# Performance work log

Hardware: AMD Instinct MI355X
Metric: run time of the kernel (lower is better)

The kernel has to match this reference:

```python
import jax, jax.numpy as jnp
import numpy as np

NODES_PER_GRAPH = 1430  # hard-coded stride in the original forward
GENE0 = 1421            # first gene node index per graph
N_HEADS = 9


def gcn_conv(x, W, b, src, dst, n):
    """PyG-style GCNConv: D^-1/2 (A+I) D^-1/2 X W + b (self-loops added)."""
    h = x @ W  # [N, out]
    ones = jnp.ones(src.shape, jnp.float32)
    deg = jax.ops.segment_sum(ones, dst, num_segments=n) + 1.0  # +1 self-loop
    dinv = jax.lax.rsqrt(deg)
    norm = dinv[src] * dinv[dst]  # [E]
    agg = jax.ops.segment_sum(norm[:, None] * h[src], dst, num_segments=n)
    agg = agg + (dinv * dinv)[:, None] * h  # self-loop contribution
    return agg + b


def setup_inputs() -> dict:
    key = jax.random.key(0)
    ks = jax.random.split(key, 8)
    n_graphs = 512
    n = NODES_PER_GRAPH * n_graphs  # 732160 nodes
    e = n * 8                        # avg degree 8
    x = jax.random.normal(ks[0], (n, 1), jnp.float32)
    edge_index = jax.random.randint(ks[1], (2, e), 0, n, jnp.int32)
    y = jnp.zeros((n_graphs * N_HEADS,), jnp.int32)  # only y.size(0) is used
    W1 = jax.random.normal(ks[2], (1, 16), jnp.float32) * 0.5
    b1 = jnp.zeros((16,), jnp.float32)
    W2 = jax.random.normal(ks[3], (16, 16), jnp.float32) * 0.25
    b2 = jnp.zeros((16,), jnp.float32)
    fw1 = jax.random.normal(ks[4], (N_HEADS, 16, 8), jnp.float32) * 0.25
    fb1 = jnp.zeros((N_HEADS, 8), jnp.float32)
    fw2 = jax.random.normal(ks[5], (N_HEADS, 8, 1), jnp.float32) * 0.35
    fb2 = jnp.zeros((N_HEADS, 1), jnp.float32)
    return {"x": x, "edge_index": edge_index, "y": y, "W1": W1, "b1": b1,
            "W2": W2, "b2": b2, "fw1": fw1, "fb1": fb1, "fw2": fw2, "fb2": fb2}


def reference(x, edge_index, y, W1, b1, W2, b2, fw1, fb1, fw2, fb2):
    n = x.shape[0]
    src, dst = edge_index[0], edge_index[1]
    h = jax.nn.relu(gcn_conv(x, W1, b1, src, dst, n))
    # F.dropout(p=0.4) treated as identity (deterministic eval reference)
    h = jax.nn.relu(gcn_conv(h, W2, b2, src, dst, n))
    n_graphs = y.shape[0] // N_HEADS
    # fused version of the per-gene gather loop: idx[g, k] = 1421+g + k*1430
    idx = (GENE0 + jnp.arange(N_HEADS)[:, None]
           + jnp.arange(n_graphs)[None, :] * NODES_PER_GRAPH)  # [9, G]
    g = h[idx]  # [9, G, 16]
    z = jax.nn.relu(jnp.einsum('gnf,gfh->gnh', g, fw1) + fb1[:, None, :])
    pred = jnp.einsum('gnh,gho->gno', z, fw2) + fb2[:, None, :]  # [9, G, 1]
    return tuple(pred[i] for i in range(N_HEADS))
```

## Files before the change

kernel.cpp:

```cpp
#include <hip/hip_runtime.h>

#define NODES 1430
#define GENE0 1421
#define NHEADS 9
#define BHIST 1024
#define GMAX 64
#define QCAP 1024

__device__ __forceinline__ float frelu(float v) { return v > 0.f ? v : 0.f; }

__global__ __launch_bounds__(BHIST, 4)
void k_hist(const int* __restrict__ esrc, const int* __restrict__ edst,
            unsigned int* __restrict__ copies,
            int* __restrict__ gene_cnt, int* __restrict__ gene_src,
            unsigned int* __restrict__ flagw,
            int e, int K, int R, int n, int hbins, int hwords) {
    extern __shared__ unsigned int lds[];
    int id = blockIdx.x;
    int k, r;
    if ((K & 7) == 0) {
        int xcd = id & 7;
        int slot = id >> 3;
        int cin = slot / R;
        k = xcd * (K >> 3) + cin;
        r = slot - cin * R;
    } else {
        k = id / R;
        r = id - k * R;
    }
    const int tid = threadIdx.x;
    {
        uint4* l4 = (uint4*)lds;
        const int hw4 = hwords >> 2;
        for (int w = tid; w < hw4; w += BHIST) l4[w] = make_uint4(0, 0, 0, 0);
    }
    __syncthreads();

    const unsigned int lo = (unsigned int)r * (unsigned int)hbins;
    const unsigned int hb = (unsigned int)hbins;
    const int e4 = e >> 2;
    const int Q = (e4 + K - 1) / K;
    const int beg = k * Q;
    const int end = min(beg + Q, e4);
    const int4* ed4 = (const int4*)edst;
    const int len = (end > beg) ? (end - beg) : 0;
    const int eighth = len >> 3;

    auto proc = [&](int4 d4) {
#pragma unroll
        for (int c = 0; c < 4; c++) {
            unsigned int d = (unsigned int)((&d4.x)[c]);
            unsigned int rel = d - lo;
            if (rel < hb)
                atomicAdd(&lds[rel >> 3], 1u << ((rel & 7u) * 4u));
        }
    };

    for (int i = tid; i < eighth; i += BHIST) {
        int j0 = beg + i;
        int4 v0 = ed4[j0];
        int4 v1 = ed4[j0 + eighth];
        int4 v2 = ed4[j0 + 2 * eighth];
        int4 v3 = ed4[j0 + 3 * eighth];
        int4 v4 = ed4[j0 + 4 * eighth];
        int4 v5 = ed4[j0 + 5 * eighth];
        int4 v6 = ed4[j0 + 6 * eighth];
        int4 v7 = ed4[j0 + 7 * eighth];
        proc(v0); proc(v1); proc(v2); proc(v3);
        proc(v4); proc(v5); proc(v6); proc(v7);
    }
    for (int i = (eighth << 3) + tid; i < len; i += BHIST) {
        proc(ed4[beg + i]);
    }

    {
        int sbeg = beg + (int)(((long long)len * r) / R);
        int send = beg + (int)(((long long)len * (r + 1)) / R);
        for (int j = sbeg + tid; j < send; j += BHIST) {
            int4 d4 = ed4[j];
#pragma unroll
            for (int c = 0; c < 4; c++) {
                unsigned int d = (unsigned int)((&d4.x)[c]);
                unsigned int graph = d / NODES;
                unsigned int pos = d - graph * NODES;
                if (pos >= GENE0) {
                    int s = esrc[4 * j + c];
                    atomicOr(&flagw[(unsigned)s >> 5], 1u << (s & 31));
                    int g = (int)(graph * NHEADS + (pos - GENE0));
                    int p = atomicAdd(gene_cnt + g, 1);
                    if (p < GMAX) gene_src[(g << 6) + p] = s;
                }
            }
        }
    }

    if (k == 0) {
        for (int j = (e4 << 2) + tid; j < e; j += BHIST) {
            unsigned int d = (unsigned int)edst[j];
            unsigned int rel = d - lo;
            if (rel < hb)
                atomicAdd(&lds[rel >> 3], 1u << ((rel & 7u) * 4u));
            if (r == 0) {
                unsigned int graph = d / NODES;
                unsigned int pos = d - graph * NODES;
                if (pos >= GENE0) {
                    int s = esrc[j];
                    atomicOr(&flagw[(unsigned)s >> 5], 1u << (s & 31));
                    int g = (int)(graph * NHEADS + (pos - GENE0));
                    int p = atomicAdd(gene_cnt + g, 1);
                    if (p < GMAX) gene_src[(g << 6) + p] = s;
                }
            }
        }
    }
    __syncthreads();
    int wlimit = (n > (int)lo) ? ((n - (int)lo + 7) >> 3) : 0;
    if (wlimit > hwords) wlimit = hwords;
    int w4 = (wlimit + 3) >> 2;
    uint4* dst4 = (uint4*)(copies + ((size_t)k * R + r) * hwords);
    const uint4* l4 = (const uint4*)lds;
    for (int w = tid; w < w4; w += BHIST) dst4[w] = l4[w];
}

__global__ void k_reduce(const unsigned int* __restrict__ copies,
                         const float* __restrict__ x,
                         float2* __restrict__ dx, float* __restrict__ t,
                         unsigned int* __restrict__ flagw,
                         int n, int K, int Wtot) {
    int w = blockIdx.x * blockDim.x + threadIdx.x;
    if (w >= Wtot) return;
    int i0 = w << 3;
    if (i0 >= n) return;
    const unsigned int M = 0x0F0F0F0Fu;
    unsigned int ev[8] = {0, 0, 0, 0, 0, 0, 0, 0};
    unsigned int od[8] = {0, 0, 0, 0, 0, 0, 0, 0};
    int k = 0;
    for (; k + 8 <= K; k += 8) {
#pragma unroll
        for (int s = 0; s < 8; s++) {
            unsigned int u = copies[(size_t)(k + s) * Wtot + w];
            ev[s] += u & M; od[s] += (u >> 4) & M;
        }
    }
    for (; k < K; k++) {
        unsigned int u = copies[(size_t)k * Wtot + w];
        ev[0] += u & M; od[0] += (u >> 4) & M;
    }
    unsigned int evn = ((ev[0] + ev[1]) + (ev[2] + ev[3])) + ((ev[4] + ev[5]) + (ev[6] + ev[7]));
    unsigned int odd = ((od[0] + od[1]) + (od[2] + od[3])) + ((od[4] + od[5]) + (od[6] + od[7]));
    float v[8];
#pragma unroll
    for (int b = 0; b < 4; b++) {
        v[2 * b]     = (float)((evn >> (8 * b)) & 0xFFu);
        v[2 * b + 1] = (float)((odd >> (8 * b)) & 0xFFu);
    }
#pragma unroll
    for (int b = 0; b < 8; b++) v[b] = rsqrtf(v[b] + 1.f);
    float4 z4 = {0.f, 0.f, 0.f, 0.f};
    if (i0 + 7 < n) {
        float4 xa = *(const float4*)(x + i0);
        float4 xb = *(const float4*)(x + i0 + 4);
        float4 p0 = {v[0], v[0] * xa.x, v[1], v[1] * xa.y};
        float4 p1 = {v[2], v[2] * xa.z, v[3], v[3] * xa.w};
        float4 p2 = {v[4], v[4] * xb.x, v[5], v[5] * xb.y};
        float4 p3 = {v[6], v[6] * xb.z, v[7], v[7] * xb.w};
        float4* dst = (float4*)(dx + i0);
        dst[0] = p0; dst[1] = p1; dst[2] = p2; dst[3] = p3;
        *(float4*)(t + i0) = z4;
        *(float4*)(t + i0 + 4) = z4;
    } else {
        for (int b = 0; b < 8; b++)
            if (i0 + b < n) {
                float xv = x[i0 + b];
                dx[i0 + b] = make_float2(v[b], v[b] * xv);
                t[i0 + b] = 0.f;
            }
    }
#pragma unroll
    for (int b = 0; b < 8; b++) {
        int i = i0 + b;
        if (i < n) {
            unsigned int graph = (unsigned int)i / NODES;
            unsigned int pos = (unsigned int)i - graph * NODES;
            if (pos >= GENE0) atomicOr(&flagw[(unsigned)i >> 5], 1u << (i & 31));
        }
    }
}

__global__ __launch_bounds__(256, 8)
void k_l1_scatter(const int* __restrict__ esrc, const int* __restrict__ edst,
                  const float2* __restrict__ dx,
                  const unsigned int* __restrict__ flagw,
                  float* __restrict__ t, int e) {
    __shared__ int2 q[QCAP];
    __shared__ int qn;
    const int tid = threadIdx.x;
    if (tid == 0) qn = 0;
    __syncthreads();

    const int4* ed4 = (const int4*)edst;
    const int4* es4 = (const int4*)esrc;
    const int e4 = e >> 2;
    const int g0 = blockIdx.x * 512;
#pragma unroll
    for (int u = 0; u < 2; u++) {
        int gi = g0 + u * 256 + tid;
        if (gi < e4) {
            int4 dd = ed4[gi];
            int4 ss = es4[gi];
#pragma unroll
            for (int c = 0; c < 4; c++) {
                int d = (&dd.x)[c];
                if ((flagw[(unsigned)d >> 5] >> (d & 31)) & 1u) {
                    int p = atomicAdd(&qn, 1);
                    if (p < QCAP) q[p] = make_int2((&ss.x)[c], d);
                    else atomicAdd(t + d, dx[(&ss.x)[c]].y);
                }
            }
        }
    }
    if (blockIdx.x == 0) {
        for (int j = (e4 << 2) + tid; j < e; j += 256) {
            int d = edst[j];
            if ((flagw[(unsigned)d >> 5] >> (d & 31)) & 1u) {
                int s = esrc[j];
                atomicAdd(t + d, dx[s].y);
            }
        }
    }
    __syncthreads();
    int m = min(qn, QCAP);
    for (int i = tid; i < m; i += 256) {
        int2 sd = q[i];
        atomicAdd(t + sd.y, dx[sd.x].y);
    }
}

__global__ void k_gene_final(const int* __restrict__ gene_cnt, const int* __restrict__ gene_src,
                             const float* __restrict__ t, const float2* __restrict__ dx,
                             const float* __restrict__ W1, const float* __restrict__ b1,
                             const float* __restrict__ W2, const float* __restrict__ b2,
                             const float* __restrict__ fw1, const float* __restrict__ fb1,
                             const float* __restrict__ fw2, const float* __restrict__ fb2,
                             float* __restrict__ out, int NG, int G) {
    int wid = (blockIdx.x * blockDim.x + threadIdx.x) >> 6;
    int lane = threadIdx.x & 63;
    if (wid >= NG) return;
    int g = wid;
    int graph = g / NHEADS;
    int head = g - graph * NHEADS;
    int node = graph * NODES + GENE0 + head;
    const int c = lane & 15;
    const int slot = lane >> 4;

    int cnt = min(gene_cnt[g], GMAX);

    float w1r[16], b1r[16], w2c[16];
#pragma unroll
    for (int kk = 0; kk < 16; kk++) {
        w1r[kk] = W1[kk];
        b1r[kk] = b1[kk];
        w2c[kk] = W2[kk * 16 + c];
    }
    float2 dn2 = dx[node];
    float tn = t[node];

    float acc = 0.f;
    const int base = g << 6;
    for (int i = slot; i < cnt; i += 8) {
        int s0 = gene_src[base + i];
        int i1 = i + 4;
        int s1 = (i1 < cnt) ? gene_src[base + i1] : -1;
        float2 a2 = dx[s0];
        float ta = t[s0];
        float2 b2v = (s1 >= 0) ? dx[s1] : make_float2(0.f, 0.f);
        float tb = (s1 >= 0) ? t[s1] : 0.f;
        {
            float us = a2.x * ta + a2.x * a2.y;
            float m = 0.f;
#pragma unroll
            for (int kk = 0; kk < 16; kk++)
                m += frelu(us * w1r[kk] + b1r[kk]) * w2c[kk];
            acc += a2.x * m;
        }
        if (s1 >= 0) {
            float us = b2v.x * tb + b2v.x * b2v.y;
            float m = 0.f;
#pragma unroll
            for (int kk = 0; kk < 16; kk++)
                m += frelu(us * w1r[kk] + b1r[kk]) * w2c[kk];
            acc += b2v.x * m;
        }
    }
    acc += __shfl_xor(acc, 16, 64);
    acc += __shfl_xor(acc, 32, 64);

    float dn = dn2.x;
    float un = dn * tn + dn * dn2.y;
    float h2 = 0.f;
#pragma unroll
    for (int kk = 0; kk < 16; kk++)
        h2 += frelu(un * w1r[kk] + b1r[kk]) * w2c[kk];
    float h = frelu(dn * acc + dn * dn * h2 + b2[c]);

    float hv[16];
#pragma unroll
    for (int c2 = 0; c2 < 16; c2++) hv[c2] = __shfl(h, c2, 64);

    int kk = lane & 7;
    float z = fb1[head * 8 + kk];
#pragma unroll
    for (int c2 = 0; c2 < 16; c2++) z += hv[c2] * fw1[head * 128 + c2 * 8 + kk];
    float term = frelu(z) * fw2[head * 8 + kk];
    term += __shfl_xor(term, 1, 64);
    term += __shfl_xor(term, 2, 64);
    term += __shfl_xor(term, 4, 64);
    if (lane == 0) out[head * G + graph] = fb2[head] + term;
}

extern "C" void kernel_launch(void* const* d_in, const int* in_sizes, int n_in,
                              void* d_out, int out_size, void* d_ws, size_t ws_size,
                              hipStream_t stream) {
    const float* x   = (const float*)d_in[0];
    const int*   ei  = (const int*)d_in[1];
    const float* W1  = (const float*)d_in[3];
    const float* b1  = (const float*)d_in[4];
    const float* W2  = (const float*)d_in[5];
    const float* b2  = (const float*)d_in[6];
    const float* fw1 = (const float*)d_in[7];
    const float* fb1 = (const float*)d_in[8];
    const float* fw2 = (const float*)d_in[9];
    const float* fb2 = (const float*)d_in[10];

    int n = in_sizes[0];
    int e = in_sizes[1] / 2;
    int G = in_sizes[2] / NHEADS;
    int NG = G * NHEADS;
    const int* esrc = ei;
    const int* edst = ei + e;

    static int HB_RT = 0;
    if (HB_RT == 0) {
        hipError_t st = hipFuncSetAttribute(
            reinterpret_cast<const void*>(k_hist),
            hipFuncAttributeMaxDynamicSharedMemorySize, 131072);
        HB_RT = (st == hipSuccess) ? 262144 : 131072;
    }
    const int HB = HB_RT;
    const int HW = HB >> 3;

    char* ws = (char*)d_ws;
    size_t off = 0;
    auto alloc = [&](size_t bytes) {
        char* p = ws + off;
        off += (bytes + 255) & ~(size_t)255;
        return p;
    };
    int*   gene_cnt      = (int*)alloc((size_t)NG * 4);
    unsigned int* flagw  = (unsigned int*)alloc((size_t)((n + 31) / 32) * 4);
    size_t zero_bytes    = off;
    int*    gene_src     = (int*)alloc((size_t)NG * GMAX * 4);
    float*  t            = (float*)alloc((size_t)n * 4);
    float2* dx           = (float2*)alloc((size_t)n * 8);
    size_t fixed         = off;

    int R = (n + HB - 1) / HB;
    size_t per_copy = (size_t)R * HW * 4;
    int K = 80;
    if (fixed + (size_t)K * per_copy > ws_size) {
        size_t avail = (ws_size > fixed) ? (ws_size - fixed) : 0;
        int kfit = (int)(avail / per_copy);
        if (kfit >= 8) kfit &= ~7;
        K = kfit < 1 ? 1 : (kfit < K ? kfit : K);
    }
    unsigned int* copies = (unsigned int*)alloc((size_t)K * per_copy);
    (void)n_in; (void)out_size;

    hipMemsetAsync(d_ws, 0, zero_bytes, stream);

    const int B = 256;
    size_t shmem = (size_t)HW * 4;
    k_hist<<<K * R, BHIST, shmem, stream>>>(esrc, edst, copies, gene_cnt, gene_src,
                                            flagw, e, K, R, n, HB, HW);
    int Wtot = R * HW;
    k_reduce<<<(Wtot + B - 1) / B, B, 0, stream>>>(copies, x, dx, t, flagw, n, K, Wtot);
    int nblk = ((e >> 2) + 511) / 512;
    k_l1_scatter<<<nblk, 256, 0, stream>>>(esrc, edst, dx, flagw, t, e);
    int waves_blocks = (NG * 64 + B - 1) / B;
    k_gene_final<<<waves_blocks, B, 0, stream>>>(gene_cnt, gene_src, t, dx,
                                                 W1, b1, W2, b2,
                                                 fw1, fb1, fw2, fb2,
                                                 (float*)d_out, NG, G);
}
```

Before: 168.8 us.

## Stage gene flag bitmap in LDS for layer-1 scatter with persistent blocks

Adds a layer-1 scatter kernel that copies the whole gene-node flag bitmap (about 92 KB for this graph) into shared memory once per block. Each of 256 blocks of 1024 threads then handles a contiguous chunk of edges and checks the flags from LDS instead of global memory. This replaces many random global bitmap loads with LDS lookups. The cost is a bitmap copy per block and large per-block LDS, which limits occupancy; the old global-memory kernel is kept as a fallback.

```diff
diff --git a/kernel.cpp b/kernel.cpp
--- a/kernel.cpp
+++ b/kernel.cpp
@@ -6,6 +6,8 @@
 #define BHIST 1024
 #define GMAX 64
 #define QCAP 1024
+#define L1B 1024
+#define L1QCAP 3072
 
 __device__ __forceinline__ float frelu(float v) { return v > 0.f ? v : 0.f; }
 
@@ -187,11 +189,79 @@
     }
 }
 
+__global__ __launch_bounds__(L1B, 4)
+void k_l1_scatter_lds(const int* __restrict__ esrc, const int* __restrict__ edst,
+                      const float2* __restrict__ dx,
+                      const unsigned int* __restrict__ flagw,
+                      float* __restrict__ t, int e, int nw) {
+    extern __shared__ unsigned int sh[];
+    unsigned int* fl = sh;
+    int2* q = (int2*)(sh + ((nw + 3) & ~3));
+    __shared__ int qn;
+    const int tid = threadIdx.x;
+    if (tid == 0) qn = 0;
+    {
+        const uint4* g4 = (const uint4*)flagw;
+        uint4* l4 = (uint4*)fl;
+        int nw4 = nw >> 2;
+        for (int w = tid; w < nw4; w += L1B) l4[w] = g4[w];
+        for (int w = (nw4 << 2) + tid; w < nw; w += L1B) fl[w] = flagw[w];
+    }
+    __syncthreads();
+
+    const int e4 = e >> 2;
+    const int nb = gridDim.x;
+    const int Q = (e4 + nb - 1) / nb;
+    const int beg = blockIdx.x * Q;
+    const int end = min(beg + Q, e4);
+    const int len = (end > beg) ? (end - beg) : 0;
+    const int4* ed4 = (const int4*)edst;
+    const int4* es4 = (const int4*)esrc;
+
+    auto test = [&](int4 dd, int4 ss) {
+#pragma unroll
+        for (int c = 0; c < 4; c++) {
+            int d = (&dd.x)[c];
+            if ((fl[(unsigned)d >> 5] >> (d & 31)) & 1u) {
+                int p = atomicAdd(&qn, 1);
+                if (p < L1QCAP) q[p] = make_int2((&ss.x)[c], d);
+                else atomicAdd(t + d, dx[(&ss.x)[c]].y);
+            }
+        }
+    };
+
+    const int quarter = len >> 2;
+    for (int i = tid; i < quarter; i += L1B) {
+        int j0 = beg + i;
+        int4 d0 = ed4[j0],               s0 = es4[j0];
+        int4 d1 = ed4[j0 + quarter],     s1 = es4[j0 + quarter];
+        int4 d2 = ed4[j0 + 2 * quarter], s2 = es4[j0 + 2 * quarter];
+        int4 d3 = ed4[j0 + 3 * quarter], s3 = es4[j0 + 3 * quarter];
+        test(d0, s0); test(d1, s1); test(d2, s2); test(d3, s3);
+    }
+    for (int i = (quarter << 2) + tid; i < len; i += L1B) {
+        test(ed4[beg + i], es4[beg + i]);
+    }
+    if (blockIdx.x == 0) {
+        for (int j = (e4 << 2) + tid; j < e; j += L1B) {
+            int d = edst[j];
+            if ((fl[(unsigned)d >> 5] >> (d & 31)) & 1u)
+                atomicAdd(t + d, dx[esrc[j]].y);
+        }
+    }
+    __syncthreads();
+    int m = min(qn, L1QCAP);
+    for (int i = tid; i < m; i += L1B) {
+        int2 sd = q[i];
+        atomicAdd(t + sd.y, dx[sd.x].y);
+    }
+}
+
 __global__ __launch_bounds__(256, 8)
-void k_l1_scatter(const int* __restrict__ esrc, const int* __restrict__ edst,
-                  const float2* __restrict__ dx,
-                  const unsigned int* __restrict__ flagw,
-                  float* __restrict__ t, int e) {
+void k_l1_scatter_g(const int* __restrict__ esrc, const int* __restrict__ edst,
+                    const float2* __restrict__ dx,
+                    const unsigned int* __restrict__ flagw,
+                    float* __restrict__ t, int e) {
     __shared__ int2 q[QCAP];
     __shared__ int qn;
     const int tid = threadIdx.x;
@@ -339,12 +409,20 @@
     const int* esrc = ei;
     const int* edst = ei + e;
 
+    int nw = (n + 31) / 32;
+    size_t l1_shmem = (size_t)((nw + 3) & ~3) * 4 + (size_t)L1QCAP * 8;
+
     static int HB_RT = 0;
+    static int L1_LDS_OK = 0;
     if (HB_RT == 0) {
         hipError_t st = hipFuncSetAttribute(
             reinterpret_cast<const void*>(k_hist),
             hipFuncAttributeMaxDynamicSharedMemorySize, 131072);
         HB_RT = (st == hipSuccess) ? 262144 : 131072;
+        hipError_t st2 = hipFuncSetAttribute(
+            reinterpret_cast<const void*>(k_l1_scatter_lds),
+            hipFuncAttributeMaxDynamicSharedMemorySize, (int)l1_shmem);
+        L1_LDS_OK = (st2 == hipSuccess && l1_shmem <= 160 * 1024) ? 1 : -1;
     }
     const int HB = HB_RT;
     const int HW = HB >> 3;
@@ -357,7 +435,7 @@
         return p;
     };
     int*   gene_cnt      = (int*)alloc((size_t)NG * 4);
-    unsigned int* flagw  = (unsigned int*)alloc((size_t)((n + 31) / 32) * 4);
+    unsigned int* flagw  = (unsigned int*)alloc((size_t)nw * 4);
     size_t zero_bytes    = off;
     int*    gene_src     = (int*)alloc((size_t)NG * GMAX * 4);
     float*  t            = (float*)alloc((size_t)n * 4);
@@ -384,8 +462,12 @@
                                             flagw, e, K, R, n, HB, HW);
     int Wtot = R * HW;
     k_reduce<<<(Wtot + B - 1) / B, B, 0, stream>>>(copies, x, dx, t, flagw, n, K, Wtot);
-    int nblk = ((e >> 2) + 511) / 512;
-    k_l1_scatter<<<nblk, 256, 0, stream>>>(esrc, edst, dx, flagw, t, e);
+    if (L1_LDS_OK == 1) {
+        k_l1_scatter_lds<<<256, L1B, l1_shmem, stream>>>(esrc, edst, dx, flagw, t, e, nw);
+    } else {
+        int nblk = ((e >> 2) + 511) / 512;
+        k_l1_scatter_g<<<nblk, 256, 0, stream>>>(esrc, edst, dx, flagw, t, e);
+    }
     int waves_blocks = (NG * 64 + B - 1) / B;
     k_gene_final<<<waves_blocks, B, 0, stream>>>(gene_cnt, gene_src, t, dx,
                                                  W1, b1, W2, b2,
```

Result: slower. 174.8 us (+3.5%).

## Fuse gene-edge collection into histogram pass and restructure layer-1 scatter

Applied to the files above, without the earlier changes.

Gene-edge detection and source recording now run inside the main histogram loop, reusing the destination values already loaded instead of rereading an edge slice. Gene nodes are no longer self-flagged in the reduce kernel; the gene node's own neighbor sum is instead computed in the final kernel from its gathered source list. The layer-1 scatter drops the LDS queue and its barrier, processes 8 int4s per thread with batched flag lookups, and atomically adds straight to global memory. This cuts the histogram kernel's extra pass and the queue overhead, at the cost of more branching inside the hot histogram loop and direct global atomics.

```diff
diff --git a/kernel.cpp b/kernel.cpp
--- a/kernel.cpp
+++ b/kernel.cpp
@@ -5,7 +5,6 @@
 #define NHEADS 9
 #define BHIST 1024
 #define GMAX 64
-#define QCAP 1024
 
 __device__ __forceinline__ float frelu(float v) { return v > 0.f ? v : 0.f; }
 
@@ -46,13 +45,23 @@
     const int len = (end > beg) ? (end - beg) : 0;
     const int eighth = len >> 3;
 
-    auto proc = [&](int4 d4) {
+    auto proc = [&](int4 d4, int j4) {
 #pragma unroll
         for (int c = 0; c < 4; c++) {
             unsigned int d = (unsigned int)((&d4.x)[c]);
             unsigned int rel = d - lo;
-            if (rel < hb)
+            if (rel < hb) {
                 atomicAdd(&lds[rel >> 3], 1u << ((rel & 7u) * 4u));
+                unsigned int graph = d / NODES;
+                unsigned int pos = d - graph * NODES;
+                if (pos >= GENE0) {
+                    int s = esrc[4 * j4 + c];
+                    atomicOr(&flagw[(unsigned)s >> 5], 1u << (s & 31));
+                    int g = (int)(graph * NHEADS + (pos - GENE0));
+                    int p = atomicAdd(gene_cnt + g, 1);
+                    if (p < GMAX) gene_src[(g << 6) + p] = s;
+                }
+            }
         }
     };
 
@@ -66,41 +75,24 @@
         int4 v5 = ed4[j0 + 5 * eighth];
         int4 v6 = ed4[j0 + 6 * eighth];
         int4 v7 = ed4[j0 + 7 * eighth];
-        proc(v0); proc(v1); proc(v2); proc(v3);
-        proc(v4); proc(v5); proc(v6); proc(v7);
+        proc(v0, j0);
+        proc(v1, j0 + eighth);
+        proc(v2, j0 + 2 * eighth);
+        proc(v3, j0 + 3 * eighth);
+        proc(v4, j0 + 4 * eighth);
+        proc(v5, j0 + 5 * eighth);
+        proc(v6, j0 + 6 * eighth);
+        proc(v7, j0 + 7 * eighth);
     }
     for (int i = (eighth << 3) + tid; i < len; i += BHIST) {
-        proc(ed4[beg + i]);
-    }
-
-    {
-        int sbeg = beg + (int)(((long long)len * r) / R);
-        int send = beg + (int)(((long long)len * (r + 1)) / R);
-        for (int j = sbeg + tid; j < send; j += BHIST) {
-            int4 d4 = ed4[j];
-#pragma unroll
-            for (int c = 0; c < 4; c++) {
-                unsigned int d = (unsigned int)((&d4.x)[c]);
-                unsigned int graph = d / NODES;
-                unsigned int pos = d - graph * NODES;
-                if (pos >= GENE0) {
-                    int s = esrc[4 * j + c];
-                    atomicOr(&flagw[(unsigned)s >> 5], 1u << (s & 31));
-                    int g = (int)(graph * NHEADS + (pos - GENE0));
-                    int p = atomicAdd(gene_cnt + g, 1);
-                    if (p < GMAX) gene_src[(g << 6) + p] = s;
-                }
-            }
-        }
-    }
-
+        proc(ed4[beg + i], beg + i);
+    }
     if (k == 0) {
         for (int j = (e4 << 2) + tid; j < e; j += BHIST) {
             unsigned int d = (unsigned int)edst[j];
             unsigned int rel = d - lo;
-            if (rel < hb)
+            if (rel < hb) {
                 atomicAdd(&lds[rel >> 3], 1u << ((rel & 7u) * 4u));
-            if (r == 0) {
                 unsigned int graph = d / NODES;
                 unsigned int pos = d - graph * NODES;
                 if (pos >= GENE0) {
@@ -125,7 +117,6 @@
 __global__ void k_reduce(const unsigned int* __restrict__ copies,
                          const float* __restrict__ x,
                          float2* __restrict__ dx, float* __restrict__ t,
-                         unsigned int* __restrict__ flagw,
                          int n, int K, int Wtot) {
     int w = blockIdx.x * blockDim.x + threadIdx.x;
     if (w >= Wtot) return;
@@ -171,19 +162,9 @@
     } else {
         for (int b = 0; b < 8; b++)
             if (i0 + b < n) {
-                float xv = x[i0 + b];
-                dx[i0 + b] = make_float2(v[b], v[b] * xv);
+                dx[i0 + b] = make_float2(v[b], v[b] * x[i0 + b]);
                 t[i0 + b] = 0.f;
             }
-    }
-#pragma unroll
-    for (int b = 0; b < 8; b++) {
-        int i = i0 + b;
-        if (i < n) {
-            unsigned int graph = (unsigned int)i / NODES;
-            unsigned int pos = (unsigned int)i - graph * NODES;
-            if (pos >= GENE0) atomicOr(&flagw[(unsigned)i >> 5], 1u << (i & 31));
-        }
     }
 }
 
@@ -192,29 +173,39 @@
                   const float2* __restrict__ dx,
                   const unsigned int* __restrict__ flagw,
                   float* __restrict__ t, int e) {
-    __shared__ int2 q[QCAP];
-    __shared__ int qn;
+    const int4* ed4 = (const int4*)edst;
+    const int e4 = e >> 2;
     const int tid = threadIdx.x;
-    if (tid == 0) qn = 0;
-    __syncthreads();
-
-    const int4* ed4 = (const int4*)edst;
-    const int4* es4 = (const int4*)esrc;
-    const int e4 = e >> 2;
-    const int g0 = blockIdx.x * 512;
-#pragma unroll
-    for (int u = 0; u < 2; u++) {
-        int gi = g0 + u * 256 + tid;
-        if (gi < e4) {
-            int4 dd = ed4[gi];
-            int4 ss = es4[gi];
+    const int base = blockIdx.x * 2048 + tid;
+
+    int4 dv[8];
+#pragma unroll
+    for (int k = 0; k < 8; k++) {
+        int j = base + k * 256;
+        dv[k] = (j < e4) ? ed4[j] : make_int4(-1, -1, -1, -1);
+    }
+    unsigned int hm[8];
+#pragma unroll
+    for (int k = 0; k < 8; k++) {
+        unsigned int m = 0;
+#pragma unroll
+        for (int c = 0; c < 4; c++) {
+            int d = (&dv[k].x)[c];
+            unsigned int widx = (d >= 0) ? ((unsigned)d >> 5) : 0u;
+            unsigned int fw = flagw[widx];
+            if (d >= 0 && ((fw >> (d & 31)) & 1u)) m |= 1u << c;
+        }
+        hm[k] = m;
+    }
+#pragma unroll
+    for (int k = 0; k < 8; k++) {
+        if (hm[k]) {
+            int j = base + k * 256;
 #pragma unroll
             for (int c = 0; c < 4; c++) {
-                int d = (&dd.x)[c];
-                if ((flagw[(unsigned)d >> 5] >> (d & 31)) & 1u) {
-                    int p = atomicAdd(&qn, 1);
-                    if (p < QCAP) q[p] = make_int2((&ss.x)[c], d);
-                    else atomicAdd(t + d, dx[(&ss.x)[c]].y);
+                if ((hm[k] >> c) & 1u) {
+                    int s = esrc[4 * j + c];
+                    atomicAdd(t + (&dv[k].x)[c], dx[s].y);
                 }
             }
         }
@@ -222,17 +213,9 @@
     if (blockIdx.x == 0) {
         for (int j = (e4 << 2) + tid; j < e; j += 256) {
             int d = edst[j];
-            if ((flagw[(unsigned)d >> 5] >> (d & 31)) & 1u) {
-                int s = esrc[j];
-                atomicAdd(t + d, dx[s].y);
-            }
-        }
-    }
-    __syncthreads();
-    int m = min(qn, QCAP);
-    for (int i = tid; i < m; i += 256) {
-        int2 sd = q[i];
-        atomicAdd(t + sd.y, dx[sd.x].y);
+            if ((flagw[(unsigned)d >> 5] >> (d & 31)) & 1u)
+                atomicAdd(t + d, dx[esrc[j]].y);
+        }
     }
 }
 
@@ -252,7 +235,6 @@
     int node = graph * NODES + GENE0 + head;
     const int c = lane & 15;
     const int slot = lane >> 4;
-
     int cnt = min(gene_cnt[g], GMAX);
 
     float w1r[16], b1r[16], w2c[16];
@@ -263,9 +245,8 @@
         w2c[kk] = W2[kk * 16 + c];
     }
     float2 dn2 = dx[node];
-    float tn = t[node];
-
-    float acc = 0.f;
+
+    float acc = 0.f, tsum = 0.f;
     const int base = g << 6;
     for (int i = slot; i < cnt; i += 8) {
         int s0 = gene_src[base + i];
@@ -275,6 +256,7 @@
         float ta = t[s0];
         float2 b2v = (s1 >= 0) ? dx[s1] : make_float2(0.f, 0.f);
         float tb = (s1 >= 0) ? t[s1] : 0.f;
+        tsum += a2.y + b2v.y;
         {
             float us = a2.x * ta + a2.x * a2.y;
             float m = 0.f;
@@ -294,9 +276,11 @@
     }
     acc += __shfl_xor(acc, 16, 64);
     acc += __shfl_xor(acc, 32, 64);
+    tsum += __shfl_xor(tsum, 16, 64);
+    tsum += __shfl_xor(tsum, 32, 64);
 
     float dn = dn2.x;
-    float un = dn * tn + dn * dn2.y;
+    float un = dn * tsum + dn * dn2.y;
     float h2 = 0.f;
 #pragma unroll
     for (int kk = 0; kk < 16; kk++)
@@ -338,6 +322,7 @@
     int NG = G * NHEADS;
     const int* esrc = ei;
     const int* edst = ei + e;
+    int nw = (n + 31) / 32;
 
     static int HB_RT = 0;
     if (HB_RT == 0) {
@@ -357,7 +342,7 @@
         return p;
     };
     int*   gene_cnt      = (int*)alloc((size_t)NG * 4);
-    unsigned int* flagw  = (unsigned int*)alloc((size_t)((n + 31) / 32) * 4);
+    unsigned int* flagw  = (unsigned int*)alloc((size_t)nw * 4);
     size_t zero_bytes    = off;
     int*    gene_src     = (int*)alloc((size_t)NG * GMAX * 4);
     float*  t            = (float*)alloc((size_t)n * 4);
@@ -383,8 +368,9 @@
     k_hist<<<K * R, BHIST, shmem, stream>>>(esrc, edst, copies, gene_cnt, gene_src,
                                             flagw, e, K, R, n, HB, HW);
     int Wtot = R * HW;
-    k_reduce<<<(Wtot + B - 1) / B, B, 0, stream>>>(copies, x, dx, t, flagw, n, K, Wtot);
-    int nblk = ((e >> 2) + 511) / 512;
+    k_reduce<<<(Wtot + B - 1) / B, B, 0, stream>>>(copies, x, dx, t, n, K, Wtot);
+    int e4 = e >> 2;
+    int nblk = (e4 + 2047) / 2048;
     k_l1_scatter<<<nblk, 256, 0, stream>>>(esrc, edst, dx, flagw, t, e);
     int waves_blocks = (NG * 64 + B - 1) / B;
     k_gene_final<<<waves_blocks, B, 0, stream>>>(gene_cnt, gene_src, t, dx,
```

Result: slower. 191.0 us (+13.1%).
